# Kernel tuning notes

Hardware: AMD Instinct MI355X
Metric: run time of the kernel (lower is better)

## Reference

```python
import jax, jax.numpy as jnp
import numpy as np

# Static ragged block structure: (num_graphs_in_bucket, n) -> block tensor (B, n, n, C)
BLOCKS = [(128, 32), (64, 48), (32, 64), (16, 96)]
C = 64
DEPTH = 2
EPS = 1e-5
N_TOTAL = sum(b * n * n for b, n in BLOCKS)  # 557056


def _mlp(h, w, b):
    # stack of DEPTH Linear(C->C) + ReLU layers (1x1 convs in the torch module)
    for d in range(w.shape[0]):
        h = jax.nn.relu(jnp.einsum('...i,oi->...o', h, w[d]) + b[d])
    return h


def _bn(h, g, b, m, v):
    # eval-mode BatchNorm1d with running stats
    return g * (h - m) * jax.lax.rsqrt(v + EPS) + b


def setup_inputs() -> dict:
    key = jax.random.key(0)
    ks = jax.random.split(key, 8)
    s = 1.0 / np.sqrt(C)

    def lin(k):
        return jax.random.normal(k, (C, C), jnp.float32) * s

    return dict(
        x=jax.random.normal(ks[0], (N_TOTAL, C), jnp.float32),
        w_m1=jax.random.normal(ks[1], (DEPTH, C, C), jnp.float32) * s,
        b_m1=jnp.zeros((DEPTH, C), jnp.float32),
        w_m2=jax.random.normal(ks[2], (DEPTH, C, C), jnp.float32) * s,
        b_m2=jnp.zeros((DEPTH, C), jnp.float32),
        W_skip=lin(ks[3]), b_skip=jnp.zeros((C,), jnp.float32),
        W_u1=lin(ks[4]), b_u1=jnp.zeros((C,), jnp.float32),
        g1=jnp.ones((C,), jnp.float32), beta1=jnp.zeros((C,), jnp.float32),
        rm1=jnp.zeros((C,), jnp.float32), rv1=jnp.ones((C,), jnp.float32),
        W_u2=lin(ks[5]), b_u2=jnp.zeros((C,), jnp.float32),
        g2=jnp.ones((C,), jnp.float32), beta2=jnp.zeros((C,), jnp.float32),
        rm2=jnp.zeros((C,), jnp.float32), rv2=jnp.ones((C,), jnp.float32),
    )


def reference(x, w_m1, b_m1, w_m2, b_m2, W_skip, b_skip,
              W_u1, b_u1, g1, beta1, rm1, rv1,
              W_u2, b_u2, g2, beta2, rm2, rv2):
    # --- ragged split -> per-block PPGN-style matmul conv -> cat ---
    hs = []
    off = 0
    for (bnum, n) in BLOCKS:
        ln = bnum * n * n
        blk = x[off:off + ln].reshape(bnum, n, n, C)  # (B, n, n, C)
        m1 = _mlp(blk, w_m1, b_m1)
        m2 = _mlp(blk, w_m2, b_m2)
        # per-channel spatial matmul over the n x n block
        h = jnp.einsum('bijc,bjkc->bikc', m1, m2)
        hs.append(h.reshape(ln, C))
        off += ln
    hs2 = jnp.concatenate(hs, 0) + (x @ W_skip.T + b_skip)
    # --- update MLP: Linear-BN-ReLU-(Dropout eval=id)-Linear-BN-ReLU + residual ---
    u = jax.nn.relu(_bn(hs2 @ W_u1.T + b_u1, g1, beta1, rm1, rv1))
    u = jax.nn.relu(_bn(u @ W_u2.T + b_u2, g2, beta2, rm2, rv2))
    return u + hs2
```

## Files before the change

### kernel.cpp

```cpp
#include <hip/hip_runtime.h>
#include <hip/hip_bf16.h>

#define NT 557056
typedef __hip_bfloat16 bf16;
typedef __attribute__((ext_vector_type(8))) short short8;
typedef __attribute__((ext_vector_type(4))) short short4v;
typedef __attribute__((ext_vector_type(4))) float f32x4;

__device__ __forceinline__ short f2bs(float f){ bf16 h = __float2bfloat16(f); return *(short*)&h; }
__device__ __forceinline__ float s2f(short s){ bf16 h = *(bf16*)&s; return __bfloat162float(h); }

__device__ __forceinline__ short8 cvt8(float4 a, float4 b){
  short8 r;
  r[0]=f2bs(a.x); r[1]=f2bs(a.y); r[2]=f2bs(a.z); r[3]=f2bs(a.w);
  r[4]=f2bs(b.x); r[5]=f2bs(b.y); r[6]=f2bs(b.z); r[7]=f2bs(b.w);
  return r;
}
__device__ __forceinline__ short8 ldfrag(const float* __restrict__ p){
  return cvt8(*(const float4*)p, *(const float4*)(p + 4));
}
__device__ __forceinline__ short8 ldfrag_s(const float* __restrict__ p, float s){
  float4 a = *(const float4*)p, b = *(const float4*)(p + 4);
  a.x*=s; a.y*=s; a.z*=s; a.w*=s; b.x*=s; b.y*=s; b.z*=s; b.w*=s;
  return cvt8(a, b);
}
#define MFMA(a,b,c) __builtin_amdgcn_mfma_f32_16x16x32_bf16(a, b, c, 0, 0, 0)

#define LS 88

__global__ __launch_bounds__(256, 2) void k1_mlp(
    const float* __restrict__ x,
    const float* __restrict__ w_m1, const float* __restrict__ b_m1,
    const float* __restrict__ w_m2, const float* __restrict__ b_m2,
    bf16* __restrict__ m1t, bf16* __restrict__ m2t)
{
  __shared__ short yL[4][2][32][LS];
  const int tid = threadIdx.x;
  const int wv = tid >> 6, lane = tid & 63, r = lane & 15, g = lane >> 4;
  const int wid = blockIdx.x * 4 + wv;

  short8 wf[4][4][2];
  #pragma unroll
  for (int cb = 0; cb < 4; ++cb)
    #pragma unroll
    for (int s = 0; s < 2; ++s) {
      const int o = (cb*16 + r)*64 + s*32 + g*8;
      wf[0][cb][s] = ldfrag(w_m1 + o);
      wf[1][cb][s] = ldfrag(w_m1 + 4096 + o);
      wf[2][cb][s] = ldfrag(w_m2 + o);
      wf[3][cb][s] = ldfrag(w_m2 + 4096 + o);
    }
  f32x4 b0v[2][4];
  float b1v[2][4];
  #pragma unroll
  for (int m = 0; m < 2; ++m) {
    const float* bb = m ? b_m2 : b_m1;
    #pragma unroll
    for (int cb = 0; cb < 4; ++cb) {
      b0v[m][cb] = *(const f32x4*)(bb + cb*16 + 4*g);
      b1v[m][cb] = bb[64 + cb*16 + r];
    }
  }

  size_t pb = (size_t)wid * 128;

  float4 xr[8];
  #pragma unroll
  for (int h = 0; h < 2; ++h) {
    const float* xp = x + (pb + h*16 + r)*64 + g*8;
    xr[4*h+0] = *(const float4*)(xp);
    xr[4*h+1] = *(const float4*)(xp + 4);
    xr[4*h+2] = *(const float4*)(xp + 32);
    xr[4*h+3] = *(const float4*)(xp + 36);
  }

  for (int t = 0; t < 4; ++t, pb += 32) {
    short8 xf[2][2];
    xf[0][0] = cvt8(xr[0], xr[1]);  xf[0][1] = cvt8(xr[2], xr[3]);
    xf[1][0] = cvt8(xr[4], xr[5]);  xf[1][1] = cvt8(xr[6], xr[7]);
    if (t < 3) {
      #pragma unroll
      for (int h = 0; h < 2; ++h) {
        const float* xp = x + (pb + 32 + h*16 + r)*64 + g*8;
        xr[4*h+0] = *(const float4*)(xp);
        xr[4*h+1] = *(const float4*)(xp + 4);
        xr[4*h+2] = *(const float4*)(xp + 32);
        xr[4*h+3] = *(const float4*)(xp + 36);
      }
    }
    #pragma unroll
    for (int m = 0; m < 2; ++m) {
      f32x4 acc[4][2];
      #pragma unroll
      for (int cb = 0; cb < 4; ++cb) { acc[cb][0] = b0v[m][cb]; acc[cb][1] = b0v[m][cb]; }
      #pragma unroll
      for (int cb = 0; cb < 4; ++cb)
        #pragma unroll
        for (int s = 0; s < 2; ++s) {
          acc[cb][0] = MFMA(wf[2*m][cb][s], xf[0][s], acc[cb][0]);
          acc[cb][1] = MFMA(wf[2*m][cb][s], xf[1][s], acc[cb][1]);
        }
      #pragma unroll
      for (int cb = 0; cb < 4; ++cb)
        #pragma unroll
        for (int th = 0; th < 2; ++th) {
          short4v v;
          #pragma unroll
          for (int q = 0; q < 4; ++q) v[q] = f2bs(fmaxf(acc[cb][th][q], 0.f));
          *(short4v*)&yL[wv][m][th*16 + r][cb*16 + 4*g] = v;
        }
      short8 af[2][2];
      #pragma unroll
      for (int th = 0; th < 2; ++th)
        #pragma unroll
        for (int s = 0; s < 2; ++s)
          af[th][s] = *(const short8*)&yL[wv][m][th*16 + r][s*32 + g*8];
      f32x4 acc2[4][2];
      #pragma unroll
      for (int cb = 0; cb < 4; ++cb) {
        const float bv = b1v[m][cb];
        acc2[cb][0] = (f32x4){bv,bv,bv,bv};
        acc2[cb][1] = (f32x4){bv,bv,bv,bv};
      }
      #pragma unroll
      for (int cb = 0; cb < 4; ++cb)
        #pragma unroll
        for (int s = 0; s < 2; ++s) {
          acc2[cb][0] = MFMA(af[0][s], wf[2*m+1][cb][s], acc2[cb][0]);
          acc2[cb][1] = MFMA(af[1][s], wf[2*m+1][cb][s], acc2[cb][1]);
        }
      bf16* op = m ? m2t : m1t;
      #pragma unroll
      for (int cb = 0; cb < 4; ++cb)
        #pragma unroll
        for (int th = 0; th < 2; ++th) {
          short4v v;
          #pragma unroll
          for (int q = 0; q < 4; ++q) v[q] = f2bs(fmaxf(acc2[cb][th][q], 0.f));
          *(short4v*)(op + (size_t)(cb*16 + r) * NT + pb + th*16 + 4*g) = v;
        }
    }
  }
}

template<int N>
__global__ __launch_bounds__(256) void k2_spatial(
    const bf16* __restrict__ m1t, const bf16* __restrict__ m2t,
    bf16* __restrict__ ht, int off)
{
  constexpr int T = N / 16;
  constexpr int SA = N + 4;
  __shared__ __align__(16) float AT[N*SA];
  __shared__ __align__(16) float Bs[N*SA];
  const int b = blockIdx.x >> 6;
  const int c = blockIdx.x & 63;
  const size_t pbase = (size_t)c * NT + (size_t)off + (size_t)b * N * N;
  const int tid = threadIdx.x;

  for (int idx = tid*4; idx < N*N; idx += 1024) {
    short4v a4 = *(const short4v*)(m1t + pbase + idx);
    short4v b4 = *(const short4v*)(m2t + pbase + idx);
    const int j = idx / N, k0 = idx - j*N;
    f32x4 bf;
    #pragma unroll
    for (int q = 0; q < 4; ++q) bf[q] = s2f(b4[q]);
    *(f32x4*)&Bs[j*SA + k0] = bf;
    #pragma unroll
    for (int q = 0; q < 4; ++q) AT[(k0+q)*SA + j] = s2f(a4[q]);
  }
  __syncthreads();

  const int ti = tid >> 4, tk = tid & 15;
  float acc[T][T];
  #pragma unroll
  for (int ii = 0; ii < T; ++ii)
    #pragma unroll
    for (int kk = 0; kk < T; ++kk) acc[ii][kk] = 0.f;

  for (int j = 0; j < N; ++j) {
    const float* ar = &AT[j*SA + ti*T];
    const float* br = &Bs[j*SA + tk*T];
    float av[T], bv[T];
    if constexpr (T == 2) {
      float2 a2 = *(const float2*)ar; av[0]=a2.x; av[1]=a2.y;
      float2 b2 = *(const float2*)br; bv[0]=b2.x; bv[1]=b2.y;
    } else if constexpr (T == 3) {
      av[0]=ar[0]; av[1]=ar[1]; av[2]=ar[2];
      bv[0]=br[0]; bv[1]=br[1]; bv[2]=br[2];
    } else if constexpr (T == 4) {
      float4 a4 = *(const float4*)ar; av[0]=a4.x; av[1]=a4.y; av[2]=a4.z; av[3]=a4.w;
      float4 b4 = *(const float4*)br; bv[0]=b4.x; bv[1]=b4.y; bv[2]=b4.z; bv[3]=b4.w;
    } else {
      #pragma unroll
      for (int p = 0; p < 3; ++p) {
        float2 a2 = *(const float2*)(ar + 2*p); av[2*p]=a2.x; av[2*p+1]=a2.y;
        float2 b2 = *(const float2*)(br + 2*p); bv[2*p]=b2.x; bv[2*p+1]=b2.y;
      }
    }
    #pragma unroll
    for (int ii = 0; ii < T; ++ii)
      #pragma unroll
      for (int kk = 0; kk < T; ++kk)
        acc[ii][kk] = fmaf(av[ii], bv[kk], acc[ii][kk]);
  }

  #pragma unroll
  for (int ii = 0; ii < T; ++ii) {
    const int row = ti*T + ii;
    bf16* dst = ht + pbase + row*N + tk*T;
    unsigned short tmp[T];
    #pragma unroll
    for (int kk = 0; kk < T; ++kk) tmp[kk] = (unsigned short)f2bs(acc[ii][kk]);
    if constexpr (T == 2) {
      *(unsigned int*)dst = (unsigned int)tmp[0] | ((unsigned int)tmp[1] << 16);
    } else if constexpr (T == 3) {
      ((unsigned short*)dst)[0] = tmp[0];
      ((unsigned short*)dst)[1] = tmp[1];
      ((unsigned short*)dst)[2] = tmp[2];
    } else if constexpr (T == 4) {
      short4v v; v[0]=(short)tmp[0]; v[1]=(short)tmp[1]; v[2]=(short)tmp[2]; v[3]=(short)tmp[3];
      *(short4v*)dst = v;
    } else {
      #pragma unroll
      for (int p = 0; p < 3; ++p)
        *((unsigned int*)dst + p) = (unsigned int)tmp[2*p] | ((unsigned int)tmp[2*p+1] << 16);
    }
  }
}

__global__ __launch_bounds__(256, 2) void k3_update(
    const float* __restrict__ x, const bf16* __restrict__ ht,
    const float* __restrict__ Wskip, const float* __restrict__ bskip,
    const float* __restrict__ Wu1, const float* __restrict__ bu1,
    const float* __restrict__ g1, const float* __restrict__ be1,
    const float* __restrict__ rm1, const float* __restrict__ rv1,
    const float* __restrict__ Wu2, const float* __restrict__ bu2,
    const float* __restrict__ g2, const float* __restrict__ be2,
    const float* __restrict__ rm2, const float* __restrict__ rv2,
    float* __restrict__ out)
{
  __shared__ short hs2L[4][32][LS];
  __shared__ short u1L[4][32][LS];
  const int tid = threadIdx.x;
  const int wv = tid >> 6, lane = tid & 63, r = lane & 15, g = lane >> 4;
  const int wid = blockIdx.x * 4 + wv;

  short8 wsk[4][2], w1f[4][2], w2f[4][2];
  float bskv[4];
  f32x4 b1c[4], b2c[4];
  #pragma unroll
  for (int cb = 0; cb < 4; ++cb) {
    const int row = cb*16 + r;
    const float s1 = g1[row] * rsqrtf(rv1[row] + 1e-5f);
    const float s2 = g2[row] * rsqrtf(rv2[row] + 1e-5f);
    #pragma unroll
    for (int s = 0; s < 2; ++s) {
      const int o = row*64 + s*32 + g*8;
      wsk[cb][s] = ldfrag(Wskip + o);
      w1f[cb][s] = ldfrag_s(Wu1 + o, s1);
      w2f[cb][s] = ldfrag_s(Wu2 + o, s2);
    }
    bskv[cb] = bskip[row];
    const int o4 = cb*16 + 4*g;
    f32x4 gg1 = *(const f32x4*)(g1 + o4),  vv1 = *(const f32x4*)(rv1 + o4);
    f32x4 mm1 = *(const f32x4*)(rm1 + o4), bb1 = *(const f32x4*)(be1 + o4);
    f32x4 u1b = *(const f32x4*)(bu1 + o4);
    f32x4 gg2 = *(const f32x4*)(g2 + o4),  vv2 = *(const f32x4*)(rv2 + o4);
    f32x4 mm2 = *(const f32x4*)(rm2 + o4), bb2 = *(const f32x4*)(be2 + o4);
    f32x4 u2b = *(const f32x4*)(bu2 + o4);
    #pragma unroll
    for (int q = 0; q < 4; ++q) {
      const float c1 = gg1[q] * rsqrtf(vv1[q] + 1e-5f);
      b1c[cb][q] = bb1[q] + (u1b[q] - mm1[q]) * c1;
      const float c2 = gg2[q] * rsqrtf(vv2[q] + 1e-5f);
      b2c[cb][q] = bb2[q] + (u2b[q] - mm2[q]) * c2;
    }
  }

  size_t pb = (size_t)wid * 128;

  float4 xr[8];
  #pragma unroll
  for (int h = 0; h < 2; ++h) {
    const float* xp = x + (pb + h*16 + r)*64 + g*8;
    xr[4*h+0] = *(const float4*)(xp);
    xr[4*h+1] = *(const float4*)(xp + 4);
    xr[4*h+2] = *(const float4*)(xp + 32);
    xr[4*h+3] = *(const float4*)(xp + 36);
  }

  for (int t = 0; t < 4; ++t, pb += 32) {
    short8 xf[2][2];
    xf[0][0] = cvt8(xr[0], xr[1]);  xf[0][1] = cvt8(xr[2], xr[3]);
    xf[1][0] = cvt8(xr[4], xr[5]);  xf[1][1] = cvt8(xr[6], xr[7]);
    if (t < 3) {
      #pragma unroll
      for (int h = 0; h < 2; ++h) {
        const float* xp = x + (pb + 32 + h*16 + r)*64 + g*8;
        xr[4*h+0] = *(const float4*)(xp);
        xr[4*h+1] = *(const float4*)(xp + 4);
        xr[4*h+2] = *(const float4*)(xp + 32);
        xr[4*h+3] = *(const float4*)(xp + 36);
      }
    }
    short4v hv[4][2];
    #pragma unroll
    for (int cb = 0; cb < 4; ++cb)
      #pragma unroll
      for (int th = 0; th < 2; ++th)
        hv[cb][th] = *(const short4v*)(ht + (size_t)(cb*16 + r) * NT + pb + th*16 + 4*g);

    f32x4 acc[4][2];
    #pragma unroll
    for (int cb = 0; cb < 4; ++cb) {
      acc[cb][0] = (f32x4){bskv[cb], bskv[cb], bskv[cb], bskv[cb]};
      acc[cb][1] = acc[cb][0];
    }
    #pragma unroll
    for (int cb = 0; cb < 4; ++cb)
      #pragma unroll
      for (int s = 0; s < 2; ++s) {
        acc[cb][0] = MFMA(xf[0][s], wsk[cb][s], acc[cb][0]);
        acc[cb][1] = MFMA(xf[1][s], wsk[cb][s], acc[cb][1]);
      }
    #pragma unroll
    for (int cb = 0; cb < 4; ++cb)
      #pragma unroll
      for (int th = 0; th < 2; ++th)
        #pragma unroll
        for (int q = 0; q < 4; ++q) acc[cb][th][q] += s2f(hv[cb][th][q]);
    #pragma unroll
    for (int cb = 0; cb < 4; ++cb)
      #pragma unroll
      for (int th = 0; th < 2; ++th)
        #pragma unroll
        for (int q = 0; q < 4; ++q)
          hs2L[wv][th*16 + 4*g + q][cb*16 + r] = f2bs(acc[cb][th][q]);
    short8 hf[2][2];
    #pragma unroll
    for (int th = 0; th < 2; ++th)
      #pragma unroll
      for (int s = 0; s < 2; ++s)
        hf[th][s] = *(const short8*)&hs2L[wv][th*16 + r][s*32 + g*8];

    f32x4 a1[4][2];
    #pragma unroll
    for (int cb = 0; cb < 4; ++cb) { a1[cb][0] = b1c[cb]; a1[cb][1] = b1c[cb]; }
    #pragma unroll
    for (int cb = 0; cb < 4; ++cb)
      #pragma unroll
      for (int s = 0; s < 2; ++s) {
        a1[cb][0] = MFMA(w1f[cb][s], hf[0][s], a1[cb][0]);
        a1[cb][1] = MFMA(w1f[cb][s], hf[1][s], a1[cb][1]);
      }
    #pragma unroll
    for (int cb = 0; cb < 4; ++cb)
      #pragma unroll
      for (int th = 0; th < 2; ++th) {
        short4v v;
        #pragma unroll
        for (int q = 0; q < 4; ++q) v[q] = f2bs(fmaxf(a1[cb][th][q], 0.f));
        *(short4v*)&u1L[wv][th*16 + r][cb*16 + 4*g] = v;
      }
    short8 uf[2][2];
    #pragma unroll
    for (int th = 0; th < 2; ++th)
      #pragma unroll
      for (int s = 0; s < 2; ++s)
        uf[th][s] = *(const short8*)&u1L[wv][th*16 + r][s*32 + g*8];

    f32x4 a2[4][2];
    #pragma unroll
    for (int cb = 0; cb < 4; ++cb) { a2[cb][0] = b2c[cb]; a2[cb][1] = b2c[cb]; }
    #pragma unroll
    for (int cb = 0; cb < 4; ++cb)
      #pragma unroll
      for (int s = 0; s < 2; ++s) {
        a2[cb][0] = MFMA(w2f[cb][s], uf[0][s], a2[cb][0]);
        a2[cb][1] = MFMA(w2f[cb][s], uf[1][s], a2[cb][1]);
      }
    #pragma unroll
    for (int cb = 0; cb < 4; ++cb)
      #pragma unroll
      for (int th = 0; th < 2; ++th) {
        short4v hres = *(const short4v*)&hs2L[wv][th*16 + r][cb*16 + 4*g];
        f32x4 res;
        #pragma unroll
        for (int q = 0; q < 4; ++q)
          res[q] = fmaxf(a2[cb][th][q], 0.f) + s2f(hres[q]);
        *(f32x4*)(out + (pb + th*16 + r)*64 + cb*16 + 4*g) = res;
      }
  }
}

extern "C" void kernel_launch(void* const* d_in, const int* in_sizes, int n_in,
                              void* d_out, int out_size, void* d_ws, size_t ws_size,
                              hipStream_t stream) {
  const float* x     = (const float*)d_in[0];
  const float* w_m1  = (const float*)d_in[1];
  const float* b_m1  = (const float*)d_in[2];
  const float* w_m2  = (const float*)d_in[3];
  const float* b_m2  = (const float*)d_in[4];
  const float* Wskip = (const float*)d_in[5];
  const float* bskip = (const float*)d_in[6];
  const float* Wu1   = (const float*)d_in[7];
  const float* bu1   = (const float*)d_in[8];
  const float* g1    = (const float*)d_in[9];
  const float* be1   = (const float*)d_in[10];
  const float* rm1   = (const float*)d_in[11];
  const float* rv1   = (const float*)d_in[12];
  const float* Wu2   = (const float*)d_in[13];
  const float* bu2   = (const float*)d_in[14];
  const float* g2    = (const float*)d_in[15];
  const float* be2   = (const float*)d_in[16];
  const float* rm2   = (const float*)d_in[17];
  const float* rv2   = (const float*)d_in[18];
  float* out = (float*)d_out;

  bf16* m1t = (bf16*)d_ws;
  bf16* m2t = m1t + (size_t)64 * NT;
  bf16* ht  = m1t;

  k1_mlp<<<1088, 256, 0, stream>>>(x, w_m1, b_m1, w_m2, b_m2, m1t, m2t);

  k2_spatial<32><<<128*64, 256, 0, stream>>>(m1t, m2t, ht, 0);
  k2_spatial<48><<< 64*64, 256, 0, stream>>>(m1t, m2t, ht, 131072);
  k2_spatial<64><<< 32*64, 256, 0, stream>>>(m1t, m2t, ht, 278528);
  k2_spatial<96><<< 16*64, 256, 0, stream>>>(m1t, m2t, ht, 409600);

  k3_update<<<1088, 256, 0, stream>>>(x, ht, Wskip, bskip,
                                      Wu1, bu1, g1, be1, rm1, rv1,
                                      Wu2, bu2, g2, be2, rm2, rv2, out);
}
```

Measured before the change: 557.4 us.

## Switch intermediate bf16 tensors to tiled 32-point-by-channel layout for coalesced access

```diff
diff --git a/kernel.cpp b/kernel.cpp
--- a/kernel.cpp
+++ b/kernel.cpp
@@ -7,6 +7,7 @@
 typedef __attribute__((ext_vector_type(4))) short short4v;
 typedef __attribute__((ext_vector_type(4))) float f32x4;
 
+
 __device__ __forceinline__ short f2bs(float f){ bf16 h = __float2bfloat16(f); return *(short*)&h; }
 __device__ __forceinline__ float s2f(short s){ bf16 h = *(bf16*)&s; return __bfloat162float(h); }
 
@@ -26,7 +27,7 @@
 }
 #define MFMA(a,b,c) __builtin_amdgcn_mfma_f32_16x16x32_bf16(a, b, c, 0, 0, 0)
 
-#define LS 88
+#define LS 72
 
 __global__ __launch_bounds__(256, 2) void k1_mlp(
     const float* __restrict__ x,
@@ -34,7 +35,7 @@
     const float* __restrict__ w_m2, const float* __restrict__ b_m2,
     bf16* __restrict__ m1t, bf16* __restrict__ m2t)
 {
-  __shared__ short yL[4][2][32][LS];
+  __shared__ short yL[4][32][LS];
   const int tid = threadIdx.x;
   const int wv = tid >> 6, lane = tid & 63, r = lane & 15, g = lane >> 4;
   const int wid = blockIdx.x * 4 + wv;
@@ -88,6 +89,7 @@
         xr[4*h+3] = *(const float4*)(xp + 36);
       }
     }
+    const size_t tbase = (pb >> 5) * 2048;
     #pragma unroll
     for (int m = 0; m < 2; ++m) {
       f32x4 acc[4][2];
@@ -107,14 +109,14 @@
           short4v v;
           #pragma unroll
           for (int q = 0; q < 4; ++q) v[q] = f2bs(fmaxf(acc[cb][th][q], 0.f));
-          *(short4v*)&yL[wv][m][th*16 + r][cb*16 + 4*g] = v;
+          *(short4v*)&yL[wv][th*16 + r][cb*16 + 4*g] = v;
         }
       short8 af[2][2];
       #pragma unroll
       for (int th = 0; th < 2; ++th)
         #pragma unroll
         for (int s = 0; s < 2; ++s)
-          af[th][s] = *(const short8*)&yL[wv][m][th*16 + r][s*32 + g*8];
+          af[th][s] = *(const short8*)&yL[wv][th*16 + r][s*32 + g*8];
       f32x4 acc2[4][2];
       #pragma unroll
       for (int cb = 0; cb < 4; ++cb) {
@@ -131,14 +133,14 @@
         }
       bf16* op = m ? m2t : m1t;
       #pragma unroll
-      for (int cb = 0; cb < 4; ++cb)
-        #pragma unroll
-        for (int th = 0; th < 2; ++th) {
-          short4v v;
+      for (int cb = 0; cb < 4; ++cb) {
+        short8 v;
+        #pragma unroll
+        for (int th = 0; th < 2; ++th)
           #pragma unroll
-          for (int q = 0; q < 4; ++q) v[q] = f2bs(fmaxf(acc2[cb][th][q], 0.f));
-          *(short4v*)(op + (size_t)(cb*16 + r) * NT + pb + th*16 + 4*g) = v;
-        }
+          for (int q = 0; q < 4; ++q) v[th*4+q] = f2bs(fmaxf(acc2[cb][th][q], 0.f));
+        *(short8*)(op + tbase + (cb*16 + r)*32 + g*8) = v;
+      }
     }
   }
 }
@@ -154,19 +156,26 @@
   __shared__ __align__(16) float Bs[N*SA];
   const int b = blockIdx.x >> 6;
   const int c = blockIdx.x & 63;
-  const size_t pbase = (size_t)c * NT + (size_t)off + (size_t)b * N * N;
+  const size_t base_tile = ((size_t)off + (size_t)b * N * N) >> 5;
   const int tid = threadIdx.x;
 
-  for (int idx = tid*4; idx < N*N; idx += 1024) {
-    short4v a4 = *(const short4v*)(m1t + pbase + idx);
-    short4v b4 = *(const short4v*)(m2t + pbase + idx);
-    const int j = idx / N, k0 = idx - j*N;
-    f32x4 bf;
-    #pragma unroll
-    for (int q = 0; q < 4; ++q) bf[q] = s2f(b4[q]);
-    *(f32x4*)&Bs[j*SA + k0] = bf;
-    #pragma unroll
-    for (int q = 0; q < 4; ++q) AT[(k0+q)*SA + j] = s2f(a4[q]);
+  for (int idx8 = tid*8; idx8 < N*N; idx8 += 2048) {
+    const size_t gaddr = (base_tile + (idx8 >> 5)) * 2048 + c*32 + (idx8 & 31);
+    short8 a8 = *(const short8*)(m1t + gaddr);
+    short8 b8 = *(const short8*)(m2t + gaddr);
+    const int gsub = (idx8 & 31) >> 3;
+    const int i0 = idx8 & ~31;
+    #pragma unroll
+    for (int th = 0; th < 2; ++th) {
+      const int i = i0 + th*16 + 4*gsub;
+      const int j = i / N, k0 = i - j*N;
+      f32x4 bq;
+      #pragma unroll
+      for (int q = 0; q < 4; ++q) bq[q] = s2f(b8[th*4+q]);
+      *(f32x4*)&Bs[j*SA + k0] = bq;
+      #pragma unroll
+      for (int q = 0; q < 4; ++q) AT[(k0+q)*SA + j] = s2f(a8[th*4+q]);
+    }
   }
   __syncthreads();
 
@@ -204,27 +213,24 @@
         acc[ii][kk] = fmaf(av[ii], bv[kk], acc[ii][kk]);
   }
 
-  #pragma unroll
-  for (int ii = 0; ii < T; ++ii) {
-    const int row = ti*T + ii;
-    bf16* dst = ht + pbase + row*N + tk*T;
-    unsigned short tmp[T];
-    #pragma unroll
-    for (int kk = 0; kk < T; ++kk) tmp[kk] = (unsigned short)f2bs(acc[ii][kk]);
-    if constexpr (T == 2) {
-      *(unsigned int*)dst = (unsigned int)tmp[0] | ((unsigned int)tmp[1] << 16);
-    } else if constexpr (T == 3) {
-      ((unsigned short*)dst)[0] = tmp[0];
-      ((unsigned short*)dst)[1] = tmp[1];
-      ((unsigned short*)dst)[2] = tmp[2];
-    } else if constexpr (T == 4) {
-      short4v v; v[0]=(short)tmp[0]; v[1]=(short)tmp[1]; v[2]=(short)tmp[2]; v[3]=(short)tmp[3];
-      *(short4v*)dst = v;
-    } else {
-      #pragma unroll
-      for (int p = 0; p < 3; ++p)
-        *((unsigned int*)dst + p) = (unsigned int)tmp[2*p] | ((unsigned int)tmp[2*p+1] << 16);
-    }
+  __syncthreads();
+  float* Cf = AT;
+  #pragma unroll
+  for (int ii = 0; ii < T; ++ii)
+    #pragma unroll
+    for (int kk = 0; kk < T; ++kk)
+      Cf[(ti*T + ii)*N + tk*T + kk] = acc[ii][kk];
+  __syncthreads();
+
+  for (int idx8 = tid*8; idx8 < N*N; idx8 += 2048) {
+    const int i0 = idx8 & ~31, gsub = (idx8 & 31) >> 3;
+    f32x4 lo = *(const f32x4*)&Cf[i0 + 4*gsub];
+    f32x4 hi = *(const f32x4*)&Cf[i0 + 16 + 4*gsub];
+    short8 v;
+    #pragma unroll
+    for (int q = 0; q < 4; ++q) { v[q] = f2bs(lo[q]); v[4+q] = f2bs(hi[q]); }
+    const size_t gaddr = (base_tile + (idx8 >> 5)) * 2048 + c*32 + (idx8 & 31);
+    *(short8*)(ht + gaddr) = v;
   }
 }
 
@@ -303,12 +309,11 @@
         xr[4*h+3] = *(const float4*)(xp + 36);
       }
     }
-    short4v hv[4][2];
-    #pragma unroll
-    for (int cb = 0; cb < 4; ++cb)
-      #pragma unroll
-      for (int th = 0; th < 2; ++th)
-        hv[cb][th] = *(const short4v*)(ht + (size_t)(cb*16 + r) * NT + pb + th*16 + 4*g);
+    const size_t tbase = (pb >> 5) * 2048;
+    short8 hv8[4];
+    #pragma unroll
+    for (int cb = 0; cb < 4; ++cb)
+      hv8[cb] = *(const short8*)(ht + tbase + (cb*16 + r)*32 + g*8);
 
     f32x4 acc[4][2];
     #pragma unroll
@@ -328,7 +333,7 @@
       #pragma unroll
       for (int th = 0; th < 2; ++th)
         #pragma unroll
-        for (int q = 0; q < 4; ++q) acc[cb][th][q] += s2f(hv[cb][th][q]);
+        for (int q = 0; q < 4; ++q) acc[cb][th][q] += s2f(hv8[cb][th*4+q]);
     #pragma unroll
     for (int cb = 0; cb < 4; ++cb)
       #pragma unroll
```

Result: slower. 568.6 us (+2.0%).
